# Kernel optimization log

Hardware: AMD Instinct MI355X
Metric: run time of the kernel (lower is better)

The kernel has to match this reference:

```python
import jax, jax.numpy as jnp
import numpy as np

B, N, D, K = 4, 256, 128, 8
H = 2 * D   # MLP hidden
F3 = 3 * D  # pair feature dim


def setup_inputs() -> dict:
    key = jax.random.key(0)
    ks = jax.random.split(key, 9)
    init = lambda k, shape: (jax.random.normal(k, shape, jnp.float32) * 0.02)
    s = jax.random.normal(ks[0], (B, N, D), jnp.float32)
    return {
        "s": s,
        "Wg1": init(ks[1], (F3, H)), "bg1": jnp.zeros((H,), jnp.float32),
        "Wg2": init(ks[2], (H, 1)),  "bg2": jnp.zeros((1,), jnp.float32),
        "Wa1": init(ks[3], (F3, H)), "ba1": jnp.zeros((H,), jnp.float32),
        "Wa2": init(ks[4], (H, 1)),  "ba2": jnp.zeros((1,), jnp.float32),
    }


def _mlp(x, W1, b1, W2, b2):
    # 2-layer MLP: Linear -> ReLU -> Linear (dropout inactive at eval)
    return jax.nn.relu(x @ W1 + b1) @ W2 + b2


def reference(s, Wg1, bg1, Wg2, bg2, Wa1, ba1, Wa2, ba2):
    b, n, d = s.shape
    si = s[:, :, None, :]                      # [B,N,1,D]
    sj = s[:, None, :, :]                      # [B,1,N,D]
    pair = jnp.concatenate([
        jnp.broadcast_to(si, (b, n, n, d)),
        jnp.broadcast_to(sj, (b, n, n, d)),
        si * sj,
    ], axis=-1)                                # [B,N,N,3D]

    # Stage 1: discrete top-K peer gating
    scores = _mlp(pair, Wg1, bg1, Wg2, bg2)[..., 0]   # [B,N,N]
    k = min(K, n)
    _, topk_idx = jax.lax.top_k(scores, k)            # [B,N,K]
    gate = jax.nn.one_hot(topk_idx, n, dtype=jnp.float32).sum(-2)  # [B,N,N] binary

    # Stage 2: soft relevance weighting over selected peers
    att_logits = _mlp(pair, Wa1, ba1, Wa2, ba2)[..., 0]            # [B,N,N]
    att_logits = jnp.where(gate > 0, att_logits, -jnp.inf)
    att_weights = jnp.nan_to_num(jax.nn.softmax(att_logits, axis=-1))

    ctx = jnp.einsum('bij,bij,bjd->bid', gate, att_weights, s)     # [B,N,D]
    return ctx, gate, att_weights
```

## Files before the change

kernel.cpp:

```cpp
#include <hip/hip_runtime.h>
#include <math.h>

#define B_ 4
#define N_ 256
#define D_ 128
#define H_ 256
#define K_ 8
#define NJP 64

typedef short v8s __attribute__((ext_vector_type(8)));
typedef float v16f __attribute__((ext_vector_type(16)));

__device__ inline void split_bf16(float x, unsigned short& hi, unsigned short& lo) {
  unsigned u = __float_as_uint(x);
  unsigned uh = u & 0xFFFF0000u;
  hi = (unsigned short)(uh >> 16);
  float r = x - __uint_as_float(uh);
  unsigned ur = __float_as_uint(r);
  ur += 0x7FFFu + ((ur >> 16) & 1u);
  lo = (unsigned short)(ur >> 16);
}

__global__ __launch_bounds__(256) void prep_all(
    const float* __restrict__ s,
    const float* __restrict__ Wg1, const float* __restrict__ bg1,
    const float* __restrict__ Wa1, const float* __restrict__ ba1,
    float* __restrict__ Ag, float* __restrict__ Aa,
    unsigned short* __restrict__ Wghi, unsigned short* __restrict__ Wglo,
    unsigned short* __restrict__ Wahi,
    unsigned short* __restrict__ Sfh, unsigned short* __restrict__ Sfl) {
  __shared__ float sh[D_];
  const int blk = blockIdx.x;
  if (blk < 1024) {
    const int b = blk >> 8, n = blk & 255, h = threadIdx.x;
    if (h < D_) sh[h] = s[(b * N_ + n) * D_ + h];
    __syncthreads();
    float ag = bg1[h], aa = ba1[h];
#pragma unroll 8
    for (int d = 0; d < D_; d++) {
      ag = fmaf(sh[d], Wg1[d * H_ + h], ag);
      aa = fmaf(sh[d], Wa1[d * H_ + h], aa);
    }
    Ag[(b * N_ + n) * H_ + h] = ag;
    Aa[(b * N_ + n) * H_ + h] = aa;
  } else if (blk < 1152) {
    const int id = blk - 1024;
    if (threadIdx.x < 64) {
      const int ks = id >> 3, tile = id & 7, lane = threadIdx.x;
      const int h = tile * 32 + (lane & 31);
      const int kbase = ks * 16 + (lane >> 5) * 8;
      const int idx0 = (id * 64 + lane) * 8;
#pragma unroll
      for (int e = 0; e < 8; e++) {
        const int k = kbase + e;
        const int f = (k < D_) ? (2 * D_ + k) : k;
        unsigned short x, y;
        split_bf16(Wg1[f * H_ + h], x, y);
        Wghi[idx0 + e] = x;
        Wglo[idx0 + e] = y;
        unsigned short xa, ya;
        split_bf16(Wa1[f * H_ + h], xa, ya);
        Wahi[idx0 + e] = xa;
      }
    }
  } else {
    const int id = blk - 1152;
    const int b = id >> 3, jt = id & 7;
    const int lane = threadIdx.x & 63, k0 = threadIdx.x >> 6;
    const int j = jt * 32 + (lane & 31);
#pragma unroll
    for (int ksl = k0; ksl < 8; ksl += 4) {
      const int d = ksl * 16 + (lane >> 5) * 8;
      const float* sp = s + (b * N_ + j) * D_ + d;
      const float4 f0 = *(const float4*)(sp);
      const float4 f1 = *(const float4*)(sp + 4);
      v8s vh, vl;
      unsigned short x, y;
      split_bf16(f0.x, x, y); vh[0] = (short)x; vl[0] = (short)y;
      split_bf16(f0.y, x, y); vh[1] = (short)x; vl[1] = (short)y;
      split_bf16(f0.z, x, y); vh[2] = (short)x; vl[2] = (short)y;
      split_bf16(f0.w, x, y); vh[3] = (short)x; vl[3] = (short)y;
      split_bf16(f1.x, x, y); vh[4] = (short)x; vl[4] = (short)y;
      split_bf16(f1.y, x, y); vh[5] = (short)x; vl[5] = (short)y;
      split_bf16(f1.z, x, y); vh[6] = (short)x; vl[6] = (short)y;
      split_bf16(f1.w, x, y); vh[7] = (short)x; vl[7] = (short)y;
      const int dst = (((b * 8 + jt) * 8 + ksl) * 64 + lane) * 8;
      *(v8s*)(Sfh + dst) = vh;
      *(v8s*)(Sfl + dst) = vl;
    }
  }
}

__device__ inline void arg_better(float v2, int i2, float& v, int& idx) {
  if (v2 > v || (v2 == v && i2 < idx)) { v = v2; idx = i2; }
}

__device__ inline int a_idx(int jl, int k) {
  return (((jl >> 5) * 8 + (k >> 4)) * 64 + ((k >> 3) & 1) * 32 + (jl & 31)) * 8
         + (k & 7);
}
#define ALO 8192

__global__ __launch_bounds__(256, 2) void score_kernel(
    const float* __restrict__ s,
    const float* __restrict__ Ag, const float* __restrict__ Aa,
    const unsigned short* __restrict__ Sfh, const unsigned short* __restrict__ Sfl,
    const unsigned short* __restrict__ Wghi, const unsigned short* __restrict__ Wglo,
    const unsigned short* __restrict__ Wahi,
    const float* __restrict__ Wg2, const float* __restrict__ bg2p,
    const float* __restrict__ Wa2, const float* __restrict__ ba2p,
    float* __restrict__ out) {
  const int b = blockIdx.x >> 8;
  const int i = blockIdx.x & 255;
  const int t = threadIdx.x;
  const int wv = t >> 6, lane = t & 63;
  const int m32 = lane & 31, half32 = lane >> 5;

  __shared__ __align__(16) unsigned short a_all[2 * ALO + 64];
  __shared__ float si_sh[D_];
  __shared__ float sc_part[8 * NJP];
  __shared__ float scg_sh[N_];
  __shared__ float attl_sh[N_];
  __shared__ float red_v[4];
  __shared__ int red_i[4];
  __shared__ int sel_list[K_];

  if (t < D_) si_sh[t] = s[(b * N_ + i) * D_ + t];

  float agv[2], w2g[2], aav[2], w2a[2];
#pragma unroll
  for (int ht = 0; ht < 2; ht++) {
    const int hg = wv * 64 + ht * 32 + m32;
    agv[ht] = Ag[(b * N_ + i) * H_ + hg];
    w2g[ht] = Wg2[hg];
    aav[ht] = Aa[(b * N_ + i) * H_ + hg];
    w2a[ht] = Wa2[hg];
  }

  const int boff = ((2 * wv) * 64 + lane) * 8;

#define MF(A_, B_v, C_) C_ = __builtin_amdgcn_mfma_f32_32x32x16_bf16(A_, B_v, C_, 0, 0, 0)

#pragma unroll 1
  for (int ph = 0; ph < 4; ph++) {
    __syncthreads();
    {
      const int jl = t >> 2, kq = t & 3;
      const int jg = b * N_ + ph * NJP + jl;
      const float* srow = s + jg * D_ + kq * 32;
      const float* sic = si_sh + kq * 32;
#pragma unroll
      for (int u = 0; u < 4; u++) {
        const float4 sv0 = *(const float4*)(srow + u * 8);
        const float4 sv1 = *(const float4*)(srow + u * 8 + 4);
        v8s vh, vl;
        unsigned short x, y;
        split_bf16(sic[u * 8 + 0] * sv0.x, x, y); vh[0] = (short)x; vl[0] = (short)y;
        split_bf16(sic[u * 8 + 1] * sv0.y, x, y); vh[1] = (short)x; vl[1] = (short)y;
        split_bf16(sic[u * 8 + 2] * sv0.z, x, y); vh[2] = (short)x; vl[2] = (short)y;
        split_bf16(sic[u * 8 + 3] * sv0.w, x, y); vh[3] = (short)x; vl[3] = (short)y;
        split_bf16(sic[u * 8 + 4] * sv1.x, x, y); vh[4] = (short)x; vl[4] = (short)y;
        split_bf16(sic[u * 8 + 5] * sv1.y, x, y); vh[5] = (short)x; vl[5] = (short)y;
        split_bf16(sic[u * 8 + 6] * sv1.z, x, y); vh[6] = (short)x; vl[6] = (short)y;
        split_bf16(sic[u * 8 + 7] * sv1.w, x, y); vh[7] = (short)x; vl[7] = (short)y;
        const int idx = a_idx(jl, kq * 32 + u * 8);
        *(v8s*)(a_all + idx) = vh;
        *(v8s*)(a_all + ALO + idx) = vl;
      }
    }
    __syncthreads();

    const unsigned short* sf_base_h = Sfh + ((b * 8 + ph * 2) * 8) * 512 + lane * 8;
    const unsigned short* sf_base_l = Sfl + ((b * 8 + ph * 2) * 8) * 512 + lane * 8;

    v16f g00, g01, g10, g11, a00, a01, a10, a11;
    g00 = g01 = g10 = g11 = (v16f)(0.f);
    a00 = a01 = a10 = a11 = (v16f)(0.f);

    {
      const unsigned short* pgh = Wghi + boff;
      const unsigned short* pgl = Wglo + boff;
      const unsigned short* pah = Wahi + boff;
      v8s bh[2][2], bl[2][2], ba[2][2];
      bh[0][0] = *(const v8s*)pgh;  bh[0][1] = *(const v8s*)(pgh + 512);
      bl[0][0] = *(const v8s*)pgl;  bl[0][1] = *(const v8s*)(pgl + 512);
      ba[0][0] = *(const v8s*)pah;  ba[0][1] = *(const v8s*)(pah + 512);
      pgh += 4096;  pgl += 4096;  pah += 4096;

      const unsigned short* ahp = a_all + lane * 8;
#pragma unroll 2
      for (int ks = 0; ks < 8; ks++) {
        const int cur = ks & 1, nxt = cur ^ 1;
        bh[nxt][0] = *(const v8s*)pgh;  bh[nxt][1] = *(const v8s*)(pgh + 512);
        bl[nxt][0] = *(const v8s*)pgl;  bl[nxt][1] = *(const v8s*)(pgl + 512);
        ba[nxt][0] = *(const v8s*)pah;  ba[nxt][1] = *(const v8s*)(pah + 512);
        pgh += 4096;  pgl += 4096;  pah += 4096;
        v8s ah0 = *(const v8s*)(ahp);
        v8s ah1 = *(const v8s*)(ahp + 4096);
        v8s al0 = *(const v8s*)(ahp + ALO);
        v8s al1 = *(const v8s*)(ahp + ALO + 4096);
        ahp += 512;
        MF(ah0, bh[cur][0], g00); MF(ah0, bh[cur][1], g01);
        MF(ah0, ba[cur][0], a00); MF(ah0, ba[cur][1], a01);
        MF(ah0, bl[cur][0], g00); MF(ah0, bl[cur][1], g01);
        MF(al0, bh[cur][0], g00); MF(al0, bh[cur][1], g01);
        MF(ah1, bh[cur][0], g10); MF(ah1, bh[cur][1], g11);
        MF(ah1, ba[cur][0], a10); MF(ah1, ba[cur][1], a11);
        MF(ah1, bl[cur][0], g10); MF(ah1, bl[cur][1], g11);
        MF(al1, bh[cur][0], g10); MF(al1, bh[cur][1], g11);
      }
      const unsigned short* sfh = sf_base_h;
      const unsigned short* sfl = sf_base_l;
#pragma unroll 2
      for (int ks = 8; ks < 16; ks++) {
        const int cur = ks & 1, nxt = cur ^ 1;
        bh[nxt][0] = *(const v8s*)pgh;  bh[nxt][1] = *(const v8s*)(pgh + 512);
        bl[nxt][0] = *(const v8s*)pgl;  bl[nxt][1] = *(const v8s*)(pgl + 512);
        ba[nxt][0] = *(const v8s*)pah;  ba[nxt][1] = *(const v8s*)(pah + 512);
        pgh += 4096;  pgl += 4096;  pah += 4096;
        v8s ah0 = *(const v8s*)(sfh);
        v8s ah1 = *(const v8s*)(sfh + 4096);
        v8s al0 = *(const v8s*)(sfl);
        v8s al1 = *(const v8s*)(sfl + 4096);
        sfh += 512;  sfl += 512;
        MF(ah0, bh[cur][0], g00); MF(ah0, bh[cur][1], g01);
        MF(ah0, ba[cur][0], a00); MF(ah0, ba[cur][1], a01);
        MF(ah0, bl[cur][0], g00); MF(ah0, bl[cur][1], g01);
        MF(al0, bh[cur][0], g00); MF(al0, bh[cur][1], g01);
        MF(ah1, bh[cur][0], g10); MF(ah1, bh[cur][1], g11);
        MF(ah1, ba[cur][0], a10); MF(ah1, ba[cur][1], a11);
        MF(ah1, bl[cur][0], g10); MF(ah1, bl[cur][1], g11);
        MF(al1, bh[cur][0], g10); MF(al1, bh[cur][1], g11);
      }
    }

    {
      float sg[32];
#pragma unroll
      for (int m = 0; m < 32; m++) sg[m] = 0.f;
#pragma unroll
      for (int r = 0; r < 16; r++) {
        sg[r]      = fmaf(fmaxf(g00[r] + agv[0], 0.f), w2g[0], sg[r]);
        sg[r]      = fmaf(fmaxf(g01[r] + agv[1], 0.f), w2g[1], sg[r]);
        sg[16 + r] = fmaf(fmaxf(g10[r] + agv[0], 0.f), w2g[0], sg[16 + r]);
        sg[16 + r] = fmaf(fmaxf(g11[r] + agv[1], 0.f), w2g[1], sg[16 + r]);
      }
#pragma unroll
      for (int m = 0; m < 32; m++) {
        float v = sg[m];
#pragma unroll
        for (int off = 1; off <= 16; off <<= 1) v += __shfl_xor(v, off, 64);
        sg[m] = v;
      }
      if (m32 == 0) {
#pragma unroll
        for (int jt = 0; jt < 2; jt++)
#pragma unroll
          for (int r = 0; r < 16; r++) {
            const int jl = jt * 32 + (r & 3) + 8 * (r >> 2) + 4 * half32;
            sc_part[wv * NJP + jl] = sg[jt * 16 + r];
          }
      }
      float sa[32];
#pragma unroll
      for (int m = 0; m < 32; m++) sa[m] = 0.f;
#pragma unroll
      for (int r = 0; r < 16; r++) {
        sa[r]      = fmaf(fmaxf(a00[r] + aav[0], 0.f), w2a[0], sa[r]);
        sa[r]      = fmaf(fmaxf(a01[r] + aav[1], 0.f), w2a[1], sa[r]);
        sa[16 + r] = fmaf(fmaxf(a10[r] + aav[0], 0.f), w2a[0], sa[16 + r]);
        sa[16 + r] = fmaf(fmaxf(a11[r] + aav[1], 0.f), w2a[1], sa[16 + r]);
      }
#pragma unroll
      for (int m = 0; m < 32; m++) {
        float v = sa[m];
#pragma unroll
        for (int off = 1; off <= 16; off <<= 1) v += __shfl_xor(v, off, 64);
        sa[m] = v;
      }
      if (m32 == 0) {
#pragma unroll
        for (int jt = 0; jt < 2; jt++)
#pragma unroll
          for (int r = 0; r < 16; r++) {
            const int jl = jt * 32 + (r & 3) + 8 * (r >> 2) + 4 * half32;
            sc_part[4 * NJP + wv * NJP + jl] = sa[jt * 16 + r];
          }
      }
    }
    __syncthreads();
    if (t < NJP) {
      scg_sh[ph * NJP + t] = sc_part[t] + sc_part[NJP + t] + sc_part[2 * NJP + t]
                           + sc_part[3 * NJP + t] + bg2p[0];
      attl_sh[ph * NJP + t] = sc_part[4 * NJP + t] + sc_part[5 * NJP + t]
                            + sc_part[6 * NJP + t] + sc_part[7 * NJP + t] + ba2p[0];
    }
  }
  __syncthreads();

  for (int k = 0; k < K_; k++) {
    float v = scg_sh[t];
    int idx = t;
#pragma unroll
    for (int off = 32; off > 0; off >>= 1) {
      const float vo = __shfl_down(v, off, 64);
      const int io = __shfl_down(idx, off, 64);
      arg_better(vo, io, v, idx);
    }
    if ((t & 63) == 0) { red_v[t >> 6] = v; red_i[t >> 6] = idx; }
    __syncthreads();
    if (t == 0) {
      float bv = red_v[0];
      int bi = red_i[0];
      for (int w = 1; w < 4; w++) arg_better(red_v[w], red_i[w], bv, bi);
      sel_list[k] = bi;
      scg_sh[bi] = -INFINITY;
    }
    __syncthreads();
  }

  bool selj = false;
#pragma unroll
  for (int k = 0; k < K_; k++) selj = selj || (sel_list[k] == t);

  if (t == 0) {
    float m = -INFINITY;
    for (int k = 0; k < K_; k++) m = fmaxf(m, attl_sh[sel_list[k]]);
    float ssum = 0.f;
    for (int k = 0; k < K_; k++) ssum += expf(attl_sh[sel_list[k]] - m);
    red_v[0] = m;
    red_v[1] = ssum;
  }
  __syncthreads();
  const float att = selj ? expf(attl_sh[t] - red_v[0]) / red_v[1] : 0.f;

  float* __restrict__ ctx_out = out;
  float* __restrict__ gate_out = out + B_ * N_ * D_;
  float* __restrict__ att_out = out + B_ * N_ * D_ + B_ * N_ * N_;

  const int row = (b * N_ + i) * N_;
  gate_out[row + t] = selj ? 1.f : 0.f;
  att_out[row + t] = att;

  __syncthreads();
  attl_sh[t] = att;
  __syncthreads();

  if (t < D_) {
    float acc2 = 0.f;
#pragma unroll
    for (int k = 0; k < K_; k++) {
      const int jj = sel_list[k];
      acc2 = fmaf(attl_sh[jj], s[(b * N_ + jj) * D_ + t], acc2);
    }
    ctx_out[(b * N_ + i) * D_ + t] = acc2;
  }
#undef MF
}

extern "C" void kernel_launch(void* const* d_in, const int* in_sizes, int n_in,
                              void* d_out, int out_size, void* d_ws, size_t ws_size,
                              hipStream_t stream) {
  const float* s   = (const float*)d_in[0];
  const float* Wg1 = (const float*)d_in[1];
  const float* bg1 = (const float*)d_in[2];
  const float* Wg2 = (const float*)d_in[3];
  const float* bg2 = (const float*)d_in[4];
  const float* Wa1 = (const float*)d_in[5];
  const float* ba1 = (const float*)d_in[6];
  const float* Wa2 = (const float*)d_in[7];
  const float* ba2 = (const float*)d_in[8];
  float* out = (float*)d_out;

  float* ws = (float*)d_ws;
  float* Ag = ws;
  float* Aa = Ag + B_ * N_ * H_;
  unsigned short* Wghi = (unsigned short*)(Aa + B_ * N_ * H_);
  unsigned short* Wglo = Wghi + 65536 + 4096;
  unsigned short* Wahi = Wglo + 65536 + 4096;
  unsigned short* Sfh  = Wahi + 65536 + 4096;
  unsigned short* Sfl  = Sfh + B_ * 32768;

  prep_all<<<dim3(1184), dim3(256), 0, stream>>>(
      s, Wg1, bg1, Wa1, ba1, Ag, Aa, Wghi, Wglo, Wahi, Sfh, Sfl);
  score_kernel<<<dim3(B_ * N_), dim3(256), 0, stream>>>(
      s, Ag, Aa, Sfh, Sfl, Wghi, Wglo, Wahi, Wg2, bg2, Wa2, ba2, out);
}
```

Measured before the change: 241.4 us.

## Split hidden dimension across eight waves per block to raise occupancy

Doubles the score kernel block to 512 threads so each wave computes 32 hidden units instead of 64, halving MFMA accumulators and B-operand registers per wave. This is meant to increase resident waves and hide memory and MFMA latency better. In exchange, each A-operand fragment (LDS and Sf global loads) is reused across half as many MFMAs, increasing load traffic. The partial-score reduction grows to 8 waves, and the top-k and output code is guarded for threads beyond N.

```diff
diff --git a/kernel.cpp b/kernel.cpp
--- a/kernel.cpp
+++ b/kernel.cpp
@@ -101,7 +101,7 @@
 }
 #define ALO 8192
 
-__global__ __launch_bounds__(256, 2) void score_kernel(
+__global__ __launch_bounds__(512, 4) void score_kernel(
     const float* __restrict__ s,
     const float* __restrict__ Ag, const float* __restrict__ Aa,
     const unsigned short* __restrict__ Sfh, const unsigned short* __restrict__ Sfl,
@@ -118,7 +118,7 @@
 
   __shared__ __align__(16) unsigned short a_all[2 * ALO + 64];
   __shared__ float si_sh[D_];
-  __shared__ float sc_part[8 * NJP];
+  __shared__ float sc_part[16 * NJP];
   __shared__ float scg_sh[N_];
   __shared__ float attl_sh[N_];
   __shared__ float red_v[4];
@@ -127,30 +127,26 @@
 
   if (t < D_) si_sh[t] = s[(b * N_ + i) * D_ + t];
 
-  float agv[2], w2g[2], aav[2], w2a[2];
-#pragma unroll
-  for (int ht = 0; ht < 2; ht++) {
-    const int hg = wv * 64 + ht * 32 + m32;
-    agv[ht] = Ag[(b * N_ + i) * H_ + hg];
-    w2g[ht] = Wg2[hg];
-    aav[ht] = Aa[(b * N_ + i) * H_ + hg];
-    w2a[ht] = Wa2[hg];
-  }
-
-  const int boff = ((2 * wv) * 64 + lane) * 8;
+  const int hg = wv * 32 + m32;
+  const int boff = (wv * 64 + lane) * 8;
 
 #define MF(A_, B_v, C_) C_ = __builtin_amdgcn_mfma_f32_32x32x16_bf16(A_, B_v, C_, 0, 0, 0)
 
 #pragma unroll 1
   for (int ph = 0; ph < 4; ph++) {
+    const float agv = Ag[(b * N_ + i) * H_ + hg];
+    const float w2g = Wg2[hg];
+    const float aav = Aa[(b * N_ + i) * H_ + hg];
+    const float w2a = Wa2[hg];
+
     __syncthreads();
     {
-      const int jl = t >> 2, kq = t & 3;
+      const int jl = t >> 3, kq = t & 7;
       const int jg = b * N_ + ph * NJP + jl;
-      const float* srow = s + jg * D_ + kq * 32;
-      const float* sic = si_sh + kq * 32;
-#pragma unroll
-      for (int u = 0; u < 4; u++) {
+      const float* srow = s + jg * D_ + kq * 16;
+      const float* sic = si_sh + kq * 16;
+#pragma unroll
+      for (int u = 0; u < 2; u++) {
         const float4 sv0 = *(const float4*)(srow + u * 8);
         const float4 sv1 = *(const float4*)(srow + u * 8 + 4);
         v8s vh, vl;
@@ -163,7 +159,7 @@
         split_bf16(sic[u * 8 + 5] * sv1.y, x, y); vh[5] = (short)x; vl[5] = (short)y;
         split_bf16(sic[u * 8 + 6] * sv1.z, x, y); vh[6] = (short)x; vl[6] = (short)y;
         split_bf16(sic[u * 8 + 7] * sv1.w, x, y); vh[7] = (short)x; vl[7] = (short)y;
-        const int idx = a_idx(jl, kq * 32 + u * 8);
+        const int idx = a_idx(jl, kq * 16 + u * 8);
         *(v8s*)(a_all + idx) = vh;
         *(v8s*)(a_all + ALO + idx) = vl;
       }
@@ -173,77 +169,64 @@
     const unsigned short* sf_base_h = Sfh + ((b * 8 + ph * 2) * 8) * 512 + lane * 8;
     const unsigned short* sf_base_l = Sfl + ((b * 8 + ph * 2) * 8) * 512 + lane * 8;
 
-    v16f g00, g01, g10, g11, a00, a01, a10, a11;
-    g00 = g01 = g10 = g11 = (v16f)(0.f);
-    a00 = a01 = a10 = a11 = (v16f)(0.f);
+    v16f g0, g1, a0, a1;
+    g0 = g1 = (v16f)(0.f);
+    a0 = a1 = (v16f)(0.f);
 
     {
       const unsigned short* pgh = Wghi + boff;
       const unsigned short* pgl = Wglo + boff;
       const unsigned short* pah = Wahi + boff;
-      v8s bh[2][2], bl[2][2], ba[2][2];
-      bh[0][0] = *(const v8s*)pgh;  bh[0][1] = *(const v8s*)(pgh + 512);
-      bl[0][0] = *(const v8s*)pgl;  bl[0][1] = *(const v8s*)(pgl + 512);
-      ba[0][0] = *(const v8s*)pah;  ba[0][1] = *(const v8s*)(pah + 512);
+      v8s bh[2], bl[2], ba[2];
+      bh[0] = *(const v8s*)pgh;
+      bl[0] = *(const v8s*)pgl;
+      ba[0] = *(const v8s*)pah;
       pgh += 4096;  pgl += 4096;  pah += 4096;
 
       const unsigned short* ahp = a_all + lane * 8;
 #pragma unroll 2
       for (int ks = 0; ks < 8; ks++) {
         const int cur = ks & 1, nxt = cur ^ 1;
-        bh[nxt][0] = *(const v8s*)pgh;  bh[nxt][1] = *(const v8s*)(pgh + 512);
-        bl[nxt][0] = *(const v8s*)pgl;  bl[nxt][1] = *(const v8s*)(pgl + 512);
-        ba[nxt][0] = *(const v8s*)pah;  ba[nxt][1] = *(const v8s*)(pah + 512);
+        bh[nxt] = *(const v8s*)pgh;
+        bl[nxt] = *(const v8s*)pgl;
+        ba[nxt] = *(const v8s*)pah;
         pgh += 4096;  pgl += 4096;  pah += 4096;
         v8s ah0 = *(const v8s*)(ahp);
         v8s ah1 = *(const v8s*)(ahp + 4096);
         v8s al0 = *(const v8s*)(ahp + ALO);
         v8s al1 = *(const v8s*)(ahp + ALO + 4096);
         ahp += 512;
-        MF(ah0, bh[cur][0], g00); MF(ah0, bh[cur][1], g01);
-        MF(ah0, ba[cur][0], a00); MF(ah0, ba[cur][1], a01);
-        MF(ah0, bl[cur][0], g00); MF(ah0, bl[cur][1], g01);
-        MF(al0, bh[cur][0], g00); MF(al0, bh[cur][1], g01);
-        MF(ah1, bh[cur][0], g10); MF(ah1, bh[cur][1], g11);
-        MF(ah1, ba[cur][0], a10); MF(ah1, ba[cur][1], a11);
-        MF(ah1, bl[cur][0], g10); MF(ah1, bl[cur][1], g11);
-        MF(al1, bh[cur][0], g10); MF(al1, bh[cur][1], g11);
-      }
-      const unsigned short* sfh = sf_base_h;
-      const unsigned short* sfl = sf_base_l;
+        MF(ah0, bh[cur], g0); MF(ah0, ba[cur], a0);
+        MF(ah0, bl[cur], g0); MF(al0, bh[cur], g0);
+        MF(ah1, bh[cur], g1); MF(ah1, ba[cur], a1);
+        MF(ah1, bl[cur], g1); MF(al1, bh[cur], g1);
+      }
 #pragma unroll 2
       for (int ks = 8; ks < 16; ks++) {
         const int cur = ks & 1, nxt = cur ^ 1;
-        bh[nxt][0] = *(const v8s*)pgh;  bh[nxt][1] = *(const v8s*)(pgh + 512);
-        bl[nxt][0] = *(const v8s*)pgl;  bl[nxt][1] = *(const v8s*)(pgl + 512);
-        ba[nxt][0] = *(const v8s*)pah;  ba[nxt][1] = *(const v8s*)(pah + 512);
+        bh[nxt] = *(const v8s*)pgh;
+        bl[nxt] = *(const v8s*)pgl;
+        ba[nxt] = *(const v8s*)pah;
         pgh += 4096;  pgl += 4096;  pah += 4096;
-        v8s ah0 = *(const v8s*)(sfh);
-        v8s ah1 = *(const v8s*)(sfh + 4096);
-        v8s al0 = *(const v8s*)(sfl);
-        v8s al1 = *(const v8s*)(sfl + 4096);
-        sfh += 512;  sfl += 512;
-        MF(ah0, bh[cur][0], g00); MF(ah0, bh[cur][1], g01);
-        MF(ah0, ba[cur][0], a00); MF(ah0, ba[cur][1], a01);
-        MF(ah0, bl[cur][0], g00); MF(ah0, bl[cur][1], g01);
-        MF(al0, bh[cur][0], g00); MF(al0, bh[cur][1], g01);
-        MF(ah1, bh[cur][0], g10); MF(ah1, bh[cur][1], g11);
-        MF(ah1, ba[cur][0], a10); MF(ah1, ba[cur][1], a11);
-        MF(ah1, bl[cur][0], g10); MF(ah1, bl[cur][1], g11);
-        MF(al1, bh[cur][0], g10); MF(al1, bh[cur][1], g11);
+        const unsigned short* nh = sf_base_h + (ks - 8) * 512;
+        const unsigned short* nl = sf_base_l + (ks - 8) * 512;
+        v8s ah0 = *(const v8s*)nh;
+        v8s ah1 = *(const v8s*)(nh + 4096);
+        v8s al0 = *(const v8s*)nl;
+        v8s al1 = *(const v8s*)(nl + 4096);
+        MF(ah0, bh[cur], g0); MF(ah0, ba[cur], a0);
+        MF(ah0, bl[cur], g0); MF(al0, bh[cur], g0);
+        MF(ah1, bh[cur], g1); MF(ah1, ba[cur], a1);
+        MF(ah1, bl[cur], g1); MF(al1, bh[cur], g1);
       }
     }
 
     {
       float sg[32];
 #pragma unroll
-      for (int m = 0; m < 32; m++) sg[m] = 0.f;
-#pragma unroll
       for (int r = 0; r < 16; r++) {
-        sg[r]      = fmaf(fmaxf(g00[r] + agv[0], 0.f), w2g[0], sg[r]);
-        sg[r]      = fmaf(fmaxf(g01[r] + agv[1], 0.f), w2g[1], sg[r]);
-        sg[16 + r] = fmaf(fmaxf(g10[r] + agv[0], 0.f), w2g[0], sg[16 + r]);
-        sg[16 + r] = fmaf(fmaxf(g11[r] + agv[1], 0.f), w2g[1], sg[16 + r]);
+        sg[r]      = fmaxf(g0[r] + agv, 0.f) * w2g;
+        sg[16 + r] = fmaxf(g1[r] + agv, 0.f) * w2g;
       }
 #pragma unroll
       for (int m = 0; m < 32; m++) {
@@ -263,13 +246,9 @@
       }
       float sa[32];
 #pragma unroll
-      for (int m = 0; m < 32; m++) sa[m] = 0.f;
-#pragma unroll
       for (int r = 0; r < 16; r++) {
-        sa[r]      = fmaf(fmaxf(a00[r] + aav[0], 0.f), w2a[0], sa[r]);
-        sa[r]      = fmaf(fmaxf(a01[r] + aav[1], 0.f), w2a[1], sa[r]);
-        sa[16 + r] = fmaf(fmaxf(a10[r] + aav[0], 0.f), w2a[0], sa[16 + r]);
-        sa[16 + r] = fmaf(fmaxf(a11[r] + aav[1], 0.f), w2a[1], sa[16 + r]);
+        sa[r]      = fmaxf(a0[r] + aav, 0.f) * w2a;
+        sa[16 + r] = fmaxf(a1[r] + aav, 0.f) * w2a;
       }
 #pragma unroll
       for (int m = 0; m < 32; m++) {
@@ -284,30 +263,35 @@
 #pragma unroll
           for (int r = 0; r < 16; r++) {
             const int jl = jt * 32 + (r & 3) + 8 * (r >> 2) + 4 * half32;
-            sc_part[4 * NJP + wv * NJP + jl] = sa[jt * 16 + r];
+            sc_part[8 * NJP + wv * NJP + jl] = sa[jt * 16 + r];
           }
       }
     }
     __syncthreads();
     if (t < NJP) {
-      scg_sh[ph * NJP + t] = sc_part[t] + sc_part[NJP + t] + sc_part[2 * NJP + t]
-                           + sc_part[3 * NJP + t] + bg2p[0];
-      attl_sh[ph * NJP + t] = sc_part[4 * NJP + t] + sc_part[5 * NJP + t]
-                            + sc_part[6 * NJP + t] + sc_part[7 * NJP + t] + ba2p[0];
+      float sG = bg2p[0], sA = ba2p[0];
+#pragma unroll
+      for (int w = 0; w < 8; w++) {
+        sG += sc_part[w * NJP + t];
+        sA += sc_part[(8 + w) * NJP + t];
+      }
+      scg_sh[ph * NJP + t] = sG;
+      attl_sh[ph * NJP + t] = sA;
     }
   }
   __syncthreads();
 
   for (int k = 0; k < K_; k++) {
-    float v = scg_sh[t];
-    int idx = t;
+    float v = -INFINITY;
+    int idx = 0;
+    if (t < N_) { v = scg_sh[t]; idx = t; }
 #pragma unroll
     for (int off = 32; off > 0; off >>= 1) {
       const float vo = __shfl_down(v, off, 64);
       const int io = __shfl_down(idx, off, 64);
       arg_better(vo, io, v, idx);
     }
-    if ((t & 63) == 0) { red_v[t >> 6] = v; red_i[t >> 6] = idx; }
+    if (t < N_ && (t & 63) == 0) { red_v[t >> 6] = v; red_i[t >> 6] = idx; }
     __syncthreads();
     if (t == 0) {
       float bv = red_v[0];
@@ -332,18 +316,20 @@
     red_v[1] = ssum;
   }
   __syncthreads();
-  const float att = selj ? expf(attl_sh[t] - red_v[0]) / red_v[1] : 0.f;
+  const float att = (t < N_ && selj) ? expf(attl_sh[t] - red_v[0]) / red_v[1] : 0.f;
 
   float* __restrict__ ctx_out = out;
   float* __restrict__ gate_out = out + B_ * N_ * D_;
   float* __restrict__ att_out = out + B_ * N_ * D_ + B_ * N_ * N_;
 
   const int row = (b * N_ + i) * N_;
-  gate_out[row + t] = selj ? 1.f : 0.f;
-  att_out[row + t] = att;
+  if (t < N_) {
+    gate_out[row + t] = selj ? 1.f : 0.f;
+    att_out[row + t] = att;
+  }
 
   __syncthreads();
-  attl_sh[t] = att;
+  if (t < N_) attl_sh[t] = att;
   __syncthreads();
 
   if (t < D_) {
@@ -383,6 +369,6 @@
 
   prep_all<<<dim3(1184), dim3(256), 0, stream>>>(
       s, Wg1, bg1, Wa1, ba1, Ag, Aa, Wghi, Wglo, Wahi, Sfh, Sfl);
-  score_kernel<<<dim3(B_ * N_), dim3(256), 0, stream>>>(
+  score_kernel<<<dim3(B_ * N_), dim3(512), 0, stream>>>(
       s, Ag, Aa, Sfh, Sfl, Wghi, Wglo, Wahi, Wg2, bg2, Wa2, ba2, out);
 }
```

Result: slower. 317.6 us (+31.6%).
